# Kernel tuning notes

Hardware: AMD Instinct MI355X
Metric: run time of the kernel (lower is better)

The kernel has to match this reference:

```python
import jax, jax.numpy as jnp
import numpy as np

N_HEAD = 16
HEAD_DIM = 64


def setup_inputs() -> dict:
    key = jax.random.key(0)
    k1, k2, k3 = jax.random.split(key, 3)
    B, T, C = 1, 4096, 1024
    x = jax.random.normal(k1, (B, T, C), dtype=jnp.float32)
    w_attn = jax.random.normal(k2, (3 * C, C), dtype=jnp.float32) * (C ** -0.5)
    w_proj = jax.random.normal(k3, (C, C), dtype=jnp.float32) * (C ** -0.5)
    return {"x": x, "w_attn": w_attn, "w_proj": w_proj}


def reference(x, w_attn, w_proj):
    B, T, C = x.shape
    H, D = N_HEAD, HEAD_DIM
    qkv = jnp.einsum('btc,fc->btf', x, w_attn)  # [B,T,3C]
    q, k, v = jnp.split(qkv, 3, axis=-1)
    # [B,H,T,D]
    q = q.reshape(B, T, H, D).transpose(0, 2, 1, 3)
    k = k.reshape(B, T, H, D).transpose(0, 2, 1, 3)
    v = v.reshape(B, T, H, D).transpose(0, 2, 1, 3)
    scale = 1.0 / (D ** 0.5)
    att = jnp.einsum('bhqd,bhkd->bhqk', q, k) * scale  # [B,H,T,T]
    causal = jnp.tril(jnp.ones((T, T), dtype=bool))
    att = jnp.where(causal[None, None], att, -jnp.inf)
    att = jax.nn.softmax(att, axis=-1)
    y = jnp.einsum('bhqk,bhkd->bhqd', att, v)  # [B,H,T,D]
    y = y.transpose(0, 2, 1, 3).reshape(B, T, C)
    return jnp.einsum('btc,oc->bto', y, w_proj)
```

## Files before the change

### kernel.cpp

```cpp
#include <hip/hip_runtime.h>

typedef unsigned short u16;
typedef __bf16 bf16x8 __attribute__((ext_vector_type(8)));
typedef float f32x4 __attribute__((ext_vector_type(4)));

__device__ __forceinline__ u16 f2bf(float f) {
  union { float f; unsigned u; } v; v.f = f;
  return (u16)((v.u + 0x7fffu + ((v.u >> 16) & 1u)) >> 16);
}

__device__ __forceinline__ unsigned pkbf(float lo, float hi) {
  union { float f; unsigned u; } a, b; a.f = lo; b.f = hi;
  return __builtin_amdgcn_perm(b.u + 0x8000u, a.u + 0x8000u, 0x07060302u);
}

__device__ __forceinline__ float fexp2(float x) {
#if __has_builtin(__builtin_amdgcn_exp2f)
  return __builtin_amdgcn_exp2f(x);
#else
  return exp2f(x);
#endif
}

__device__ __forceinline__ void gld16(const u16* g, u16* l) {
  __builtin_amdgcn_global_load_lds(
      (const __attribute__((address_space(1))) void*)g,
      (__attribute__((address_space(3))) void*)l, 16, 0, 0);
}

__global__ __launch_bounds__(256) void cvt3(
    const float* __restrict__ x, const float* __restrict__ wa,
    const float* __restrict__ wp, u16* __restrict__ xb,
    u16* __restrict__ wab, u16* __restrict__ wpb)
{
  int b = blockIdx.x;
  const float* in; u16* out; int i;
  if (b < 2048)      { in = x;  out = xb;  i = b * 256 + threadIdx.x; }
  else if (b < 3584) { in = wa; out = wab; i = (b - 2048) * 256 + threadIdx.x; }
  else               { in = wp; out = wpb; i = (b - 3584) * 256 + threadIdx.x; }
  const float* p = in + (size_t)i * 8;
  float4 a = *(const float4*)p, c = *(const float4*)(p + 4);
  uint4 o;
  o.x = pkbf(a.x, a.y); o.y = pkbf(a.z, a.w);
  o.z = pkbf(c.x, c.y); o.w = pkbf(c.z, c.w);
  *(uint4*)&out[(size_t)i * 8] = o;
}

template<bool COUT_F32, bool VSPLIT>
__global__ __launch_bounds__(256, 3) void gemm_lds(
    const u16* __restrict__ A, const u16* __restrict__ B, void* __restrict__ C,
    u16* __restrict__ C2, int M, int N, int K, int ldc)
{
  __shared__ u16 S[9216];
  u16* As = S;
  u16* Bs = S + 4096;
  const int tid  = threadIdx.x;
  const int wave = tid >> 6, lane = tid & 63;
  const int quad = lane >> 4, ln = lane & 15;
  const int m0 = blockIdx.y * 128, n0 = blockIdx.x * 128;
  const int wm = (wave >> 1) * 64, wn = (wave & 1) * 64;

  const int srow = wave * 32 + (lane >> 2);
  const int scol = (lane & 3) * 8;

  f32x4 acc[4][4] = {};

  for (int k0 = 0; k0 < K; k0 += 32) {
    __syncthreads();
    const u16* ga = A + (size_t)(m0 + srow) * K + k0 + scol;
    const u16* gb = B + (size_t)(n0 + srow) * K + k0 + scol;
    gld16(ga,                  As + wave * 1024);
    gld16(ga + (size_t)16 * K, As + wave * 1024 + 512);
    gld16(gb,                  Bs + wave * 1024);
    gld16(gb + (size_t)16 * K, Bs + wave * 1024 + 512);
    __syncthreads();

    bf16x8 af[4], bfr[4];
#pragma unroll
    for (int i = 0; i < 4; ++i) af[i]  = *(const bf16x8*)&As[(wm + i * 16 + ln) * 32 + quad * 8];
#pragma unroll
    for (int j = 0; j < 4; ++j) bfr[j] = *(const bf16x8*)&Bs[(wn + j * 16 + ln) * 32 + quad * 8];
#pragma unroll
    for (int i = 0; i < 4; ++i)
#pragma unroll
      for (int j = 0; j < 4; ++j)
        acc[i][j] = __builtin_amdgcn_mfma_f32_16x16x32_bf16(af[i], bfr[j], acc[i][j], 0, 0, 0);
  }

  if constexpr (VSPLIT) {
    if (n0 >= 2048) {
      u16 (*Cs)[72] = (u16(*)[72])S;
      __syncthreads();
#pragma unroll
      for (int c = 0; c < 2; ++c) {
        if ((wave >> 1) == c) {
#pragma unroll
          for (int i = 0; i < 4; ++i)
#pragma unroll
            for (int j = 0; j < 4; ++j)
#pragma unroll
              for (int r = 0; r < 4; ++r) {
                int pos = (i >> 1) * 32 + (quad * 4 + r) * 2 + (i & 1);
                Cs[wn + j * 16 + ln][pos] = f2bf(acc[i][j][r]);
              }
        }
        __syncthreads();
        {
          int nl = tid >> 1, mseg = (tid & 1) * 32;
#pragma unroll
          for (int s2 = 0; s2 < 4; ++s2) {
            uint4 v4 = *(const uint4*)&Cs[nl][mseg + s2 * 8];
            *(uint4*)&C2[(size_t)(n0 - 2048 + nl) * 4096 + m0 + c * 64 + mseg + s2 * 8] = v4;
          }
        }
        __syncthreads();
      }
      return;
    }
  }

#pragma unroll
  for (int i = 0; i < 4; ++i)
#pragma unroll
    for (int j = 0; j < 4; ++j)
#pragma unroll
      for (int r = 0; r < 4; ++r) {
        int m = m0 + wm + i * 16 + quad * 4 + r;
        int n = n0 + wn + j * 16 + ln;
        if constexpr (COUT_F32)
          ((float*)C)[(size_t)m * ldc + n] = acc[i][j][r];
        else
          ((u16*)C)[(size_t)m * ldc + n] = f2bf(acc[i][j][r]);
      }
}

template<bool F32>
__device__ __forceinline__ void stage8(u16* dst, const void* base, size_t off) {
  if constexpr (F32) {
    const float* p = (const float*)base + off;
    float4 a = *(const float4*)p;
    float4 b = *(const float4*)(p + 4);
    uint4 q;
    q.x = pkbf(a.x, a.y); q.y = pkbf(a.z, a.w);
    q.z = pkbf(b.x, b.y); q.w = pkbf(b.z, b.w);
    *(uint4*)dst = q;
  } else {
    *(uint4*)dst = *(const uint4*)((const u16*)base + off);
  }
}

template<bool AF32, bool BF32, bool COUT_F32, bool VSPLIT>
__global__ __launch_bounds__(256) void gemm_bt(
    const void* __restrict__ A, const void* __restrict__ B, void* __restrict__ C,
    u16* __restrict__ C2, int M, int N, int K, int ldc)
{
  __shared__ u16 As[128][40];
  __shared__ u16 Bs[128][40];
  const int tid  = threadIdx.x;
  const int wave = tid >> 6, lane = tid & 63;
  const int quad = lane >> 4, ln = lane & 15;
  const int m0 = blockIdx.y * 128, n0 = blockIdx.x * 128;
  const int wm = (wave >> 1) * 64, wn = (wave & 1) * 64;

  f32x4 acc[4][4] = {};

  for (int k0 = 0; k0 < K; k0 += 32) {
    __syncthreads();
#pragma unroll
    for (int i = 0; i < 2; ++i) {
      int idx = tid + i * 256;
      int row = idx >> 2, seg = (idx & 3) * 8;
      stage8<AF32>(&As[row][seg], A, (size_t)(m0 + row) * K + k0 + seg);
      stage8<BF32>(&Bs[row][seg], B, (size_t)(n0 + row) * K + k0 + seg);
    }
    __syncthreads();
    bf16x8 af[4], bfr[4];
#pragma unroll
    for (int i = 0; i < 4; ++i) af[i]  = *(const bf16x8*)&As[wm + i * 16 + ln][quad * 8];
#pragma unroll
    for (int j = 0; j < 4; ++j) bfr[j] = *(const bf16x8*)&Bs[wn + j * 16 + ln][quad * 8];
#pragma unroll
    for (int i = 0; i < 4; ++i)
#pragma unroll
      for (int j = 0; j < 4; ++j)
        acc[i][j] = __builtin_amdgcn_mfma_f32_16x16x32_bf16(af[i], bfr[j], acc[i][j], 0, 0, 0);
  }

  if constexpr (VSPLIT) {
    if (n0 >= 2048) {
      __shared__ u16 Cs[128][72];
#pragma unroll
      for (int c = 0; c < 2; ++c) {
        if ((wave >> 1) == c) {
#pragma unroll
          for (int i = 0; i < 4; ++i)
#pragma unroll
            for (int j = 0; j < 4; ++j)
#pragma unroll
              for (int r = 0; r < 4; ++r) {
                int pos = (i >> 1) * 32 + (quad * 4 + r) * 2 + (i & 1);
                Cs[wn + j * 16 + ln][pos] = f2bf(acc[i][j][r]);
              }
        }
        __syncthreads();
        {
          int nl = tid >> 1, mseg = (tid & 1) * 32;
#pragma unroll
          for (int s2 = 0; s2 < 4; ++s2) {
            uint4 v4 = *(const uint4*)&Cs[nl][mseg + s2 * 8];
            *(uint4*)&C2[(size_t)(n0 - 2048 + nl) * 4096 + m0 + c * 64 + mseg + s2 * 8] = v4;
          }
        }
        __syncthreads();
      }
      return;
    }
  }

#pragma unroll
  for (int i = 0; i < 4; ++i)
#pragma unroll
    for (int j = 0; j < 4; ++j)
#pragma unroll
      for (int r = 0; r < 4; ++r) {
        int m = m0 + wm + i * 16 + quad * 4 + r;
        int n = n0 + wn + j * 16 + ln;
        if constexpr (COUT_F32)
          ((float*)C)[(size_t)m * ldc + n] = acc[i][j][r];
        else
          ((u16*)C)[(size_t)m * ldc + n] = f2bf(acc[i][j][r]);
      }
}

struct StageRegs { uint4 k0, k1, v0, v1; };

__device__ __forceinline__ StageRegs attn_stage_load(
    const u16* __restrict__ qk, const u16* __restrict__ vT,
    int h, int kbase, int tid) {
  StageRegs s;
  {
    int key = tid >> 2, seg = (tid & 3) * 16;
    const u16* kp = qk + (size_t)(kbase + key) * 2048 + 1024 + h * 64 + seg;
    s.k0 = *(const uint4*)kp;
    s.k1 = *(const uint4*)(kp + 8);
  }
  {
    int kh = tid >> 7, d = (tid >> 1) & 63, sg = (tid & 1) * 16;
    const u16* vp = vT + (size_t)(h * 64 + d) * 4096 + kbase + kh * 32 + sg;
    s.v0 = *(const uint4*)vp;
    s.v1 = *(const uint4*)(vp + 8);
  }
  return s;
}

__global__ __launch_bounds__(256, 2) void attn_fwd(
    const u16* __restrict__ qk, const u16* __restrict__ vT, u16* __restrict__ y)
{
  __shared__ u16 Ks[2][2][64][40];
  __shared__ u16 Vt[2][2][64][40];
  __shared__ u16 Ps[4][2][2][16][36];

  const int tid  = threadIdx.x;
  const int wave = tid >> 6, lane = tid & 63;
  const int quad = lane >> 4, ln = lane & 15;
  const int bx = blockIdx.x;
  const int qt = (bx < 256) ? (31 - (bx >> 4)) : ((bx - 256) >> 4);
  const int h  = bx & 15;
  const float C1 = 0.18033688f;

  const int sq0[2] = { qt * 128 + wave * 32, qt * 128 + wave * 32 + 16 };

  bf16x8 qa[2][2];
#pragma unroll
  for (int s = 0; s < 2; ++s) {
    const u16* qrow = qk + (size_t)(sq0[s] + ln) * 2048 + h * 64;
    qa[s][0] = *(const bf16x8*)(qrow + quad * 8);
    qa[s][1] = *(const bf16x8*)(qrow + 32 + quad * 8);
  }

  f32x4 o[2][4] = {};
  float l_i[2][4] = {};

  StageRegs st = attn_stage_load(qk, vT, h, 0, tid);
  const int ktmax = 2 * qt + 1;
  int b = 0;
  for (int kt = 0; kt <= ktmax; ++kt, b ^= 1) {
    {
      int key = tid >> 2, seg = (tid & 3) * 16;
      int kh = seg >> 5, off = seg & 31;
      *(uint4*)&Ks[b][kh][key][off]     = st.k0;
      *(uint4*)&Ks[b][kh][key][off + 8] = st.k1;
      int vh = tid >> 7, d = (tid >> 1) & 63, sg = (tid & 1) * 16;
      *(uint4*)&Vt[b][vh][d][sg]     = st.v0;
      *(uint4*)&Vt[b][vh][d][sg + 8] = st.v1;
    }
    __syncthreads();
    if (kt < ktmax) st = attn_stage_load(qk, vT, h, (kt + 1) * 64, tid);

    bf16x8 kf[2][4], vb[2][4];
#pragma unroll
    for (int hf = 0; hf < 2; ++hf)
#pragma unroll
      for (int c = 0; c < 4; ++c) {
        kf[hf][c] = *(const bf16x8*)&Ks[b][hf][c * 16 + ln][quad * 8];
        vb[hf][c] = *(const bf16x8*)&Vt[b][hf][c * 16 + ln][quad * 8];
      }

    bool act[2];
#pragma unroll
    for (int s = 0; s < 2; ++s) act[s] = (kt * 64 <= sq0[s] + 15);

#pragma unroll
    for (int s = 0; s < 2; ++s) {
      if (!act[s]) continue;
      f32x4 sv[4];
#pragma unroll
      for (int c = 0; c < 4; ++c) {
        f32x4 z = {0.f, 0.f, 0.f, 0.f};
        z = __builtin_amdgcn_mfma_f32_16x16x32_bf16(qa[s][0], kf[0][c], z, 0, 0, 0);
        z = __builtin_amdgcn_mfma_f32_16x16x32_bf16(qa[s][1], kf[1][c], z, 0, 0, 0);
        sv[c] = z;
      }
      float p[4][4];
      if (kt * 64 + 63 > sq0[s]) {
        const int rowb = sq0[s] + quad * 4;
#pragma unroll
        for (int c = 0; c < 4; ++c) {
          int col = kt * 64 + c * 16 + ln;
#pragma unroll
          for (int r = 0; r < 4; ++r) {
            float arg = (col > rowb + r) ? -200.0f : fmaf(sv[c][r], C1, -46.0f);
            p[c][r] = fexp2(arg);
          }
        }
      } else {
#pragma unroll
        for (int c = 0; c < 4; ++c)
#pragma unroll
          for (int r = 0; r < 4; ++r)
            p[c][r] = fexp2(fmaf(sv[c][r], C1, -46.0f));
      }
#pragma unroll
      for (int r = 0; r < 4; ++r)
        l_i[s][r] += (p[0][r] + p[1][r]) + (p[2][r] + p[3][r]);
#pragma unroll
      for (int r = 0; r < 4; ++r)
#pragma unroll
        for (int H = 0; H < 2; ++H)
          *(unsigned*)&Ps[wave][s][H][quad * 4 + r][ln * 2] = pkbf(p[2 * H][r], p[2 * H + 1][r]);
    }

    __asm__ volatile("s_waitcnt lgkmcnt(0)" ::: "memory");
#pragma unroll
    for (int s = 0; s < 2; ++s) {
      if (!act[s]) continue;
      bf16x8 pa0 = *(const bf16x8*)&Ps[wave][s][0][ln][quad * 8];
      bf16x8 pa1 = *(const bf16x8*)&Ps[wave][s][1][ln][quad * 8];
#pragma unroll
      for (int dt = 0; dt < 4; ++dt) {
        f32x4 z = o[s][dt];
        z = __builtin_amdgcn_mfma_f32_16x16x32_bf16(pa0, vb[0][dt], z, 0, 0, 0);
        z = __builtin_amdgcn_mfma_f32_16x16x32_bf16(pa1, vb[1][dt], z, 0, 0, 0);
        o[s][dt] = z;
      }
    }
  }

#pragma unroll
  for (int s = 0; s < 2; ++s) {
#pragma unroll
    for (int r = 0; r < 4; ++r) {
#pragma unroll
      for (int off = 8; off > 0; off >>= 1) l_i[s][r] += __shfl_xor(l_i[s][r], off, 16);
    }
#pragma unroll
    for (int r = 0; r < 4; ++r) {
      float inv = 1.0f / l_i[s][r];
      int rowg = sq0[s] + quad * 4 + r;
#pragma unroll
      for (int dt = 0; dt < 4; ++dt)
        y[(size_t)rowg * 1024 + h * 64 + dt * 16 + ln] = f2bf(o[s][dt][r] * inv);
    }
  }
}

extern "C" void kernel_launch(void* const* d_in, const int* in_sizes, int n_in,
                              void* d_out, int out_size, void* d_ws, size_t ws_size,
                              hipStream_t stream) {
  const float* x      = (const float*)d_in[0];
  const float* w_attn = (const float*)d_in[1];
  const float* w_proj = (const float*)d_in[2];

  char* ws = (char*)d_ws;
  u16* qk = (u16*)ws;
  u16* vT = (u16*)(ws + (16u << 20));

  if (ws_size >= (size_t)(40u << 20)) {
    u16* wpb = (u16*)(ws + (24u << 20));
    u16* xb  = (u16*)(ws + (26u << 20));
    u16* wab = (u16*)(ws + (34u << 20));
    u16* y   = (u16*)(ws + (26u << 20));

    cvt3<<<4096, 256, 0, stream>>>(x, w_attn, w_proj, xb, wab, wpb);
    gemm_lds<false, true><<<dim3(24, 32), 256, 0, stream>>>(
        xb, wab, qk, vT, 4096, 3072, 1024, 2048);
    attn_fwd<<<dim3(512), 256, 0, stream>>>(qk, vT, y);
    gemm_lds<true, false><<<dim3(8, 32), 256, 0, stream>>>(
        y, wpb, d_out, nullptr, 4096, 1024, 1024, 1024);
  } else {
    u16* y = (u16*)(ws + (24u << 20));
    gemm_bt<true, true, false, true><<<dim3(24, 32), 256, 0, stream>>>(
        x, w_attn, qk, vT, 4096, 3072, 1024, 2048);
    attn_fwd<<<dim3(512), 256, 0, stream>>>(qk, vT, y);
    gemm_bt<false, true, true, false><<<dim3(8, 32), 256, 0, stream>>>(
        y, w_proj, d_out, nullptr, 4096, 1024, 1024, 1024);
  }
}
```

Measured before the change: 217.8 us.

## Keep attention probabilities in registers via transposed MFMA, add 64-wide projection GEMM

The attention kernel now computes S^T = K·Q^T so each lane's score outputs already form the B-operand layout for the P·V MFMA. This drops the LDS round trip for P, the lgkmcnt wait and the per-row shuffle reductions. The V-transposed store layout in the QKV GEMM is permuted to match the new operand order. The block-to-qtile mapping is simplified, and the output projection uses a new 128x64 tile GEMM with twice as many blocks to fill more CUs. The risk is that the smaller GEMM tiles lower data reuse per block.

```diff
diff --git a/kernel.cpp b/kernel.cpp
--- a/kernel.cpp
+++ b/kernel.cpp
@@ -27,6 +27,7 @@
       (const __attribute__((address_space(1))) void*)g,
       (__attribute__((address_space(3))) void*)l, 16, 0, 0);
 }
+
 
 __global__ __launch_bounds__(256) void cvt3(
     const float* __restrict__ x, const float* __restrict__ wa,
@@ -100,7 +101,7 @@
             for (int j = 0; j < 4; ++j)
 #pragma unroll
               for (int r = 0; r < 4; ++r) {
-                int pos = (i >> 1) * 32 + (quad * 4 + r) * 2 + (i & 1);
+                int pos = (i >> 1) * 32 + quad * 8 + (i & 1) * 4 + r;
                 Cs[wn + j * 16 + ln][pos] = f2bf(acc[i][j][r]);
               }
         }
@@ -123,6 +124,62 @@
   for (int i = 0; i < 4; ++i)
 #pragma unroll
     for (int j = 0; j < 4; ++j)
+#pragma unroll
+      for (int r = 0; r < 4; ++r) {
+        int m = m0 + wm + i * 16 + quad * 4 + r;
+        int n = n0 + wn + j * 16 + ln;
+        if constexpr (COUT_F32)
+          ((float*)C)[(size_t)m * ldc + n] = acc[i][j][r];
+        else
+          ((u16*)C)[(size_t)m * ldc + n] = f2bf(acc[i][j][r]);
+      }
+}
+
+template<bool COUT_F32>
+__global__ __launch_bounds__(256, 2) void gemm_n64(
+    const u16* __restrict__ A, const u16* __restrict__ B, void* __restrict__ C,
+    int M, int N, int K, int ldc)
+{
+  __shared__ u16 S[6144];
+  u16* As = S;
+  u16* Bs = S + 4096;
+  const int tid  = threadIdx.x;
+  const int wave = tid >> 6, lane = tid & 63;
+  const int quad = lane >> 4, ln = lane & 15;
+  const int m0 = blockIdx.y * 128, n0 = blockIdx.x * 64;
+  const int wm = (wave >> 1) * 64, wn = (wave & 1) * 32;
+
+  const int srowA = wave * 32 + (lane >> 2);
+  const int srowB = wave * 16 + (lane >> 2);
+  const int scol  = (lane & 3) * 8;
+
+  f32x4 acc[4][2] = {};
+
+  for (int k0 = 0; k0 < K; k0 += 32) {
+    __syncthreads();
+    const u16* ga = A + (size_t)(m0 + srowA) * K + k0 + scol;
+    const u16* gb = B + (size_t)(n0 + srowB) * K + k0 + scol;
+    gld16(ga,                  As + wave * 1024);
+    gld16(ga + (size_t)16 * K, As + wave * 1024 + 512);
+    gld16(gb,                  Bs + wave * 512);
+    __syncthreads();
+
+    bf16x8 af[4], bfr[2];
+#pragma unroll
+    for (int i = 0; i < 4; ++i) af[i]  = *(const bf16x8*)&As[(wm + i * 16 + ln) * 32 + quad * 8];
+#pragma unroll
+    for (int j = 0; j < 2; ++j) bfr[j] = *(const bf16x8*)&Bs[(wn + j * 16 + ln) * 32 + quad * 8];
+#pragma unroll
+    for (int i = 0; i < 4; ++i)
+#pragma unroll
+      for (int j = 0; j < 2; ++j)
+        acc[i][j] = __builtin_amdgcn_mfma_f32_16x16x32_bf16(af[i], bfr[j], acc[i][j], 0, 0, 0);
+  }
+
+#pragma unroll
+  for (int i = 0; i < 4; ++i)
+#pragma unroll
+    for (int j = 0; j < 2; ++j)
 #pragma unroll
       for (int r = 0; r < 4; ++r) {
         int m = m0 + wm + i * 16 + quad * 4 + r;
@@ -198,7 +255,7 @@
             for (int j = 0; j < 4; ++j)
 #pragma unroll
               for (int r = 0; r < 4; ++r) {
-                int pos = (i >> 1) * 32 + (quad * 4 + r) * 2 + (i & 1);
+                int pos = (i >> 1) * 32 + quad * 8 + (i & 1) * 4 + r;
                 Cs[wn + j * 16 + ln][pos] = f2bf(acc[i][j][r]);
               }
         }
@@ -258,13 +315,12 @@
 {
   __shared__ u16 Ks[2][2][64][40];
   __shared__ u16 Vt[2][2][64][40];
-  __shared__ u16 Ps[4][2][2][16][36];
 
   const int tid  = threadIdx.x;
   const int wave = tid >> 6, lane = tid & 63;
   const int quad = lane >> 4, ln = lane & 15;
   const int bx = blockIdx.x;
-  const int qt = (bx < 256) ? (31 - (bx >> 4)) : ((bx - 256) >> 4);
+  const int qt = 31 - (bx >> 4);
   const int h  = bx & 15;
   const float C1 = 0.18033688f;
 
@@ -279,7 +335,7 @@
   }
 
   f32x4 o[2][4] = {};
-  float l_i[2][4] = {};
+  float l_i[2] = {0.f, 0.f};
 
   StageRegs st = attn_stage_load(qk, vT, h, 0, tid);
   const int ktmax = 2 * qt + 1;
@@ -310,57 +366,59 @@
 #pragma unroll
     for (int s = 0; s < 2; ++s) act[s] = (kt * 64 <= sq0[s] + 15);
 
+    bf16x8 pb[2][2];
 #pragma unroll
     for (int s = 0; s < 2; ++s) {
       if (!act[s]) continue;
       f32x4 sv[4];
 #pragma unroll
-      for (int c = 0; c < 4; ++c) {
+      for (int t = 0; t < 4; ++t) {
         f32x4 z = {0.f, 0.f, 0.f, 0.f};
-        z = __builtin_amdgcn_mfma_f32_16x16x32_bf16(qa[s][0], kf[0][c], z, 0, 0, 0);
-        z = __builtin_amdgcn_mfma_f32_16x16x32_bf16(qa[s][1], kf[1][c], z, 0, 0, 0);
-        sv[c] = z;
+        z = __builtin_amdgcn_mfma_f32_16x16x32_bf16(kf[0][t], qa[s][0], z, 0, 0, 0);
+        z = __builtin_amdgcn_mfma_f32_16x16x32_bf16(kf[1][t], qa[s][1], z, 0, 0, 0);
+        sv[t] = z;
       }
       float p[4][4];
       if (kt * 64 + 63 > sq0[s]) {
-        const int rowb = sq0[s] + quad * 4;
-#pragma unroll
-        for (int c = 0; c < 4; ++c) {
-          int col = kt * 64 + c * 16 + ln;
+        const int qr = sq0[s] + ln;
+#pragma unroll
+        for (int t = 0; t < 4; ++t) {
+          int keyb = kt * 64 + t * 16 + quad * 4;
 #pragma unroll
           for (int r = 0; r < 4; ++r) {
-            float arg = (col > rowb + r) ? -200.0f : fmaf(sv[c][r], C1, -46.0f);
-            p[c][r] = fexp2(arg);
+            float arg = (keyb + r > qr) ? -200.0f : fmaf(sv[t][r], C1, -46.0f);
+            p[t][r] = fexp2(arg);
           }
         }
       } else {
 #pragma unroll
-        for (int c = 0; c < 4; ++c)
+        for (int t = 0; t < 4; ++t)
 #pragma unroll
           for (int r = 0; r < 4; ++r)
-            p[c][r] = fexp2(fmaf(sv[c][r], C1, -46.0f));
-      }
-#pragma unroll
-      for (int r = 0; r < 4; ++r)
-        l_i[s][r] += (p[0][r] + p[1][r]) + (p[2][r] + p[3][r]);
-#pragma unroll
-      for (int r = 0; r < 4; ++r)
-#pragma unroll
-        for (int H = 0; H < 2; ++H)
-          *(unsigned*)&Ps[wave][s][H][quad * 4 + r][ln * 2] = pkbf(p[2 * H][r], p[2 * H + 1][r]);
-    }
-
-    __asm__ volatile("s_waitcnt lgkmcnt(0)" ::: "memory");
+            p[t][r] = fexp2(fmaf(sv[t][r], C1, -46.0f));
+      }
+#pragma unroll
+      for (int t = 0; t < 4; ++t)
+        l_i[s] += (p[t][0] + p[t][1]) + (p[t][2] + p[t][3]);
+#pragma unroll
+      for (int H = 0; H < 2; ++H) {
+        union { unsigned u[4]; bf16x8 v; } pk;
+        pk.u[0] = pkbf(p[2 * H][0],     p[2 * H][1]);
+        pk.u[1] = pkbf(p[2 * H][2],     p[2 * H][3]);
+        pk.u[2] = pkbf(p[2 * H + 1][0], p[2 * H + 1][1]);
+        pk.u[3] = pkbf(p[2 * H + 1][2], p[2 * H + 1][3]);
+        pb[s][H] = pk.v;
+      }
+    }
+
 #pragma unroll
     for (int s = 0; s < 2; ++s) {
       if (!act[s]) continue;
-      bf16x8 pa0 = *(const bf16x8*)&Ps[wave][s][0][ln][quad * 8];
-      bf16x8 pa1 = *(const bf16x8*)&Ps[wave][s][1][ln][quad * 8];
 #pragma unroll
       for (int dt = 0; dt < 4; ++dt) {
         f32x4 z = o[s][dt];
-        z = __builtin_amdgcn_mfma_f32_16x16x32_bf16(pa0, vb[0][dt], z, 0, 0, 0);
-        z = __builtin_amdgcn_mfma_f32_16x16x32_bf16(pa1, vb[1][dt], z, 0, 0, 0);
+        z = __builtin_amdgcn_mfma_f32_16x16x32_bf16(vb[0][dt], pb[s][0], z, 0, 0, 0);
+        z = __builtin_amdgcn_mfma_f32_16x16x32_bf16(vb[1][dt], pb[s][1], z, 0, 0, 0);
         o[s][dt] = z;
       }
     }
@@ -368,19 +426,15 @@
 
 #pragma unroll
   for (int s = 0; s < 2; ++s) {
-#pragma unroll
-    for (int r = 0; r < 4; ++r) {
-#pragma unroll
-      for (int off = 8; off > 0; off >>= 1) l_i[s][r] += __shfl_xor(l_i[s][r], off, 16);
-    }
-#pragma unroll
-    for (int r = 0; r < 4; ++r) {
-      float inv = 1.0f / l_i[s][r];
-      int rowg = sq0[s] + quad * 4 + r;
-#pragma unroll
-      for (int dt = 0; dt < 4; ++dt)
-        y[(size_t)rowg * 1024 + h * 64 + dt * 16 + ln] = f2bf(o[s][dt][r] * inv);
-    }
+    l_i[s] += __shfl_xor(l_i[s], 16);
+    l_i[s] += __shfl_xor(l_i[s], 32);
+    float inv = 1.0f / l_i[s];
+    int rowg = sq0[s] + ln;
+#pragma unroll
+    for (int dt = 0; dt < 4; ++dt)
+#pragma unroll
+      for (int r = 0; r < 4; ++r)
+        y[(size_t)rowg * 1024 + h * 64 + dt * 16 + quad * 4 + r] = f2bf(o[s][dt][r] * inv);
   }
 }
 
@@ -405,8 +459,8 @@
     gemm_lds<false, true><<<dim3(24, 32), 256, 0, stream>>>(
         xb, wab, qk, vT, 4096, 3072, 1024, 2048);
     attn_fwd<<<dim3(512), 256, 0, stream>>>(qk, vT, y);
-    gemm_lds<true, false><<<dim3(8, 32), 256, 0, stream>>>(
-        y, wpb, d_out, nullptr, 4096, 1024, 1024, 1024);
+    gemm_n64<true><<<dim3(16, 32), 256, 0, stream>>>(
+        y, wpb, d_out, 4096, 1024, 1024, 1024);
   } else {
     u16* y = (u16*)(ws + (24u << 20));
     gemm_bt<true, true, false, true><<<dim3(24, 32), 256, 0, stream>>>(
```

After: 210.3 us. -3.4%, faster.
